# Kernel tuning notes

Measured on AMD Instinct MI355X. Metric: run time of the kernel, lower is better.

Reference implementation:

```python
import jax, jax.numpy as jnp
import numpy as np

S, B, DI, DH, NH = 1024, 64, 256, 256, 4  # seq_len, batch, input_dim, hidden_dim, attn_heads


def _lin(k, fan_in, shape):
    bound = 1.0 / np.sqrt(fan_in)
    return jax.random.uniform(k, shape, jnp.float32, -bound, bound)


def setup_inputs() -> dict:
    key = jax.random.key(0)
    ks = jax.random.split(key, 14)
    inp = {"inputs": jax.random.normal(ks[0], (S, B, DI), jnp.float32)}
    names = ["Wf", "bf", "Wi", "bi", "Wg", "bg", "Wo", "bo"]
    for j in range(4):
        inp[names[2 * j]] = _lin(ks[1 + 2 * j], DI + DH, (DI + DH, DH))
        inp[names[2 * j + 1]] = _lin(ks[2 + 2 * j], DI + DH, (DH,))
    inp["in_proj_w"] = _lin(ks[9], DH, (DH, 3 * DH))
    inp["in_proj_b"] = jnp.zeros((3 * DH,), jnp.float32)
    inp["out_proj_w"] = _lin(ks[10], DH, (DH, DH))
    inp["out_proj_b"] = jnp.zeros((DH,), jnp.float32)
    return inp


def reference(inputs, Wf, bf, Wi, bi, Wg, bg, Wo, bo,
              in_proj_w, in_proj_b, out_proj_w, out_proj_b):
    D = Wf.shape[1]
    bsz = inputs.shape[1]

    def step(carry, x):
        hx, cx = carry
        comb = jnp.concatenate([x, hx], axis=-1)  # [B, DI+DH]
        f = jax.nn.sigmoid(comb @ Wf + bf)
        i = jax.nn.sigmoid(comb @ Wi + bi)
        g = jnp.tanh(comb @ Wg + bg)
        o = jax.nn.sigmoid(comb @ Wo + bo)
        cx = f * cx + i * g
        hx = o * jnp.tanh(cx)
        return (hx, cx), hx

    init = (jnp.zeros((bsz, D), inputs.dtype), jnp.zeros((bsz, D), inputs.dtype))
    (hx, cx), Hseq = jax.lax.scan(step, init, inputs)  # Hseq: [S, B, D]

    # Faithful quirk: nn.MultiheadAttention(batch_first=True) is fed the
    # time-major [S, B, D] tensor, so S acts as the batch dim and attention
    # runs over the B (batch) axis.
    dh = D // NH
    qkv = Hseq @ in_proj_w + in_proj_b  # [S, B, 3D]
    q, k, v = jnp.split(qkv, 3, axis=-1)
    q = q.reshape(S_, bsz, NH, dh) if False else q.reshape(q.shape[0], bsz, NH, dh)
    k = k.reshape(k.shape[0], bsz, NH, dh)
    v = v.reshape(v.shape[0], bsz, NH, dh)
    scale = float(1.0 / np.sqrt(dh))
    scores = jnp.einsum('sqhd,skhd->shqk', q, k) * scale  # [S, H, B, B]
    attn = jax.nn.softmax(scores, axis=-1)
    ctx = jnp.einsum('shqk,skhd->sqhd', attn, v).reshape(Hseq.shape)
    attn_out = ctx @ out_proj_w + out_proj_b
    fused = Hseq + attn_out
    return (fused, (hx, cx))
```

## Files before the change

kernel.cpp:

```cpp
#include <hip/hip_runtime.h>
#include <cstdint>
#include <cstddef>


typedef _Float16 f16;
typedef __attribute__((ext_vector_type(2))) _Float16 half2v;
typedef __attribute__((ext_vector_type(4))) _Float16 half4v;
typedef __attribute__((ext_vector_type(8))) _Float16 half8v;
typedef __attribute__((ext_vector_type(4))) float   float4v;
typedef __attribute__((ext_vector_type(2))) float   float2v;

static __device__ __forceinline__ half2v u2h(unsigned u) {
  union { unsigned u; half2v h; } x; x.u = u; return x.h;
}
static __device__ __forceinline__ float sigm(float x) {
  return 1.0f / (1.0f + __expf(-x));
}
static __device__ __forceinline__ float tanh_fast(float x) {
  x = fminf(15.0f, fmaxf(-15.0f, x));
  float e = __expf(2.0f * x);
  return (e - 1.0f) / (e + 1.0f);
}
static __device__ __forceinline__ const float* selW(int g, const float* a, const float* b,
                                                    const float* c, const float* d) {
  return g == 0 ? a : (g == 1 ? b : (g == 2 ? c : d));
}

static __device__ __forceinline__ void wg_barrier_lds() {
  __builtin_amdgcn_sched_barrier(0);
  asm volatile("s_waitcnt lgkmcnt(0)" ::: "memory");
  __builtin_amdgcn_s_barrier();
  __builtin_amdgcn_sched_barrier(0);
}

__global__ void prep_k(const float* __restrict__ Wf, const float* __restrict__ Wi,
                       const float* __restrict__ Wg_, const float* __restrict__ Wo,
                       const float* __restrict__ bf, const float* __restrict__ bi,
                       const float* __restrict__ bg_, const float* __restrict__ bo,
                       const float* __restrict__ inpw, const float* __restrict__ outpw,
                       f16* __restrict__ wscan, f16* __restrict__ wxt,
                       f16* __restrict__ inpj, f16* __restrict__ outpj,
                       float* __restrict__ bias4)
{
  const int total = 262144 + 262144 + 196608 + 65536 + 1024;
  for (int e = blockIdx.x * blockDim.x + threadIdx.x; e < total; e += gridDim.x * blockDim.x) {
    int x = e;
    if (x < 262144) {
      int c = x >> 8, k = x & 255;
      int g = c >> 8, j = c & 255;
      const float* W = selW(g, Wf, Wi, Wg_, Wo);
      wscan[x] = (f16)W[(256 + k) * 256 + j];
      continue;
    }
    x -= 262144;
    if (x < 262144) {
      int j = x & 7, lane = (x >> 3) & 63, kstep = (x >> 9) & 7, ntile = x >> 12;
      int n = ntile * 16 + (lane & 15);
      int k = kstep * 32 + ((lane >> 4) & 3) * 8 + j;
      int g = n >> 8, jj = n & 255;
      const float* W = selW(g, Wf, Wi, Wg_, Wo);
      wxt[x] = (f16)W[k * 256 + jj];
      continue;
    }
    x -= 262144;
    if (x < 196608) {
      int j = x & 7, lane = (x >> 3) & 63, kstep = (x >> 9) & 7, ntile = x >> 12;
      int n = ntile * 16 + (lane & 15);
      int k = kstep * 32 + ((lane >> 4) & 3) * 8 + j;
      inpj[x] = (f16)inpw[k * 768 + n];
      continue;
    }
    x -= 196608;
    if (x < 65536) {
      int j = x & 7, lane = (x >> 3) & 63, kstep = (x >> 9) & 7, ntile = x >> 12;
      int n = ntile * 16 + (lane & 15);
      int k = kstep * 32 + ((lane >> 4) & 3) * 8 + j;
      outpj[x] = (f16)outpw[k * 256 + n];
      continue;
    }
    x -= 65536;
    {
      int g = x >> 8, j = x & 255;
      const float* bp = selW(g, bf, bi, bg_, bo);
      bias4[x] = bp[j];
    }
  }
}

__global__ void cvt_x_k(const float4v* __restrict__ X, half4v* __restrict__ Xh)
{
  int i = blockIdx.x * 256 + threadIdx.x;
  float4v v = X[i];
  half4v h;
  h.x = (f16)v.x; h.y = (f16)v.y; h.z = (f16)v.z; h.w = (f16)v.w;
  Xh[i] = h;
}

template<int NTOT, bool OUT_EPI>
__global__ __launch_bounds__(256, 2) void gemm_k(const f16* __restrict__ A,
    const f16* __restrict__ Bf, const float* __restrict__ bias,
    f16* __restrict__ Oh, float* __restrict__ Of)
{
  __shared__ f16 Al[8192];
  const int tid = threadIdx.x;
  const int lane = tid & 63;
  const int wm = (tid >> 7) & 1;
  const int wn = (tid >> 6) & 1;
  const int m0 = blockIdx.y * 128, n0 = blockIdx.x * 128;

  float4v acc[4][4];
  #pragma unroll
  for (int i = 0; i < 4; ++i)
    #pragma unroll
    for (int j = 0; j < 4; ++j) { acc[i][j].x = 0.f; acc[i][j].y = 0.f; acc[i][j].z = 0.f; acc[i][j].w = 0.f; }

  #pragma unroll 1
  for (int kc = 0; kc < 4; ++kc) {
    __syncthreads();
    #pragma unroll
    for (int p = 0; p < 4; ++p) {
      int m = p * 32 + (tid >> 3);
      int kk = (tid & 7) * 8;
      half8v v = *(const half8v*)(A + (size_t)(m0 + m) * 256 + kc * 64 + kk);
      int lt = ((kk >> 3) & 3) * 16 + (m & 15);
      *(half8v*)(Al + (((m >> 4) * 2 + (kk >> 5)) * 64 + lt) * 8) = v;
    }
    __syncthreads();
    half8v bfr[4][2], afr[4][2];
    #pragma unroll
    for (int i = 0; i < 4; ++i) {
      int NT = (n0 >> 4) + wn * 4 + i;
      #pragma unroll
      for (int ks = 0; ks < 2; ++ks)
        bfr[i][ks] = *(const half8v*)(Bf + (size_t)((NT * 8 + kc * 2 + ks) * 64 + lane) * 8);
    }
    #pragma unroll
    for (int i = 0; i < 4; ++i) {
      int MT = wm * 4 + i;
      #pragma unroll
      for (int ks = 0; ks < 2; ++ks)
        afr[i][ks] = *(const half8v*)(Al + ((MT * 2 + ks) * 64 + lane) * 8);
    }
    #pragma unroll
    for (int ks = 0; ks < 2; ++ks)
      #pragma unroll
      for (int i = 0; i < 4; ++i)
        #pragma unroll
        for (int jn = 0; jn < 4; ++jn)
          acc[i][jn] = __builtin_amdgcn_mfma_f32_16x16x32_f16(afr[i][ks], bfr[jn][ks], acc[i][jn], 0, 0, 0);
  }

  const int r0 = (lane >> 4) * 4, cn = lane & 15;
  #pragma unroll
  for (int i = 0; i < 4; ++i) {
    #pragma unroll
    for (int jn = 0; jn < 4; ++jn) {
      int n = n0 + wn * 64 + jn * 16 + cn;
      float bv = bias[n];
      int mb = m0 + wm * 64 + i * 16 + r0;
      #pragma unroll
      for (int r = 0; r < 4; ++r) {
        float v = acc[i][jn][r] + bv;
        size_t off = (size_t)(mb + r) * NTOT + n;
        if constexpr (OUT_EPI) Of[off] = v + Of[off];
        else                   Oh[off] = (f16)v;
      }
    }
  }
}

__global__ __launch_bounds__(512, 2) void scan_k(const f16* __restrict__ Xp,
    const f16* __restrict__ Wscan, float* __restrict__ dout, f16* __restrict__ Hh)
{
  extern __shared__ unsigned smem[];
  unsigned* wtl = smem;
  f16* hxs = (f16*)(smem + 32768);
  float* gts = (float*)(smem + 32768 + 128);
  const int tid = threadIdx.x;
  const int b = blockIdx.x;
  const int c0 = tid << 1;
  const unsigned* W32 = (const unsigned*)Wscan;

  unsigned wv[192];
  #pragma unroll
  for (int r = 0; r < 96; ++r) {
    wv[r]      = W32[c0 * 128 + r];
    wv[96 + r] = W32[(c0 + 1) * 128 + r];
  }
  for (int e = tid; e < 32768; e += 512) {
    int r2 = e >> 10, c = e & 1023;
    wtl[(r2 << 10) + c] = W32[c * 128 + 96 + r2];
  }
  if (tid < 128) ((unsigned*)hxs)[tid] = 0u;
  float cx = 0.0f, hx_keep = 0.0f;
  const int gate = tid >> 7;
  __syncthreads();

  const unsigned* xptr = (const unsigned*)Xp + (size_t)b * 512 + tid;
  unsigned xp_cur = xptr[0];

  #pragma unroll 1
  for (int t = 0; t < 1024; ++t) {
    unsigned xp_nxt = 0u;
    if (t + 1 < 1024) xp_nxt = xptr[(size_t)(t + 1) << 15];

    float a0 = 0.0f, a1 = 0.0f;
    #pragma unroll
    for (int ch = 0; ch < 24; ++ch) {
      half8v h8 = *(const half8v*)(hxs + ch * 8);
      const half2v* hp = (const half2v*)&h8;
      #pragma unroll
      for (int z = 0; z < 4; ++z) {
        int r = ch * 4 + z;
        a0 = __builtin_amdgcn_fdot2(hp[z], u2h(wv[r]), a0, false);
        a1 = __builtin_amdgcn_fdot2(hp[z], u2h(wv[96 + r]), a1, false);
      }
    }
    #pragma unroll
    for (int ch = 0; ch < 8; ++ch) {
      half8v h8 = *(const half8v*)(hxs + 192 + ch * 8);
      const half2v* hp = (const half2v*)&h8;
      #pragma unroll
      for (int z = 0; z < 4; ++z) {
        int r2 = ch * 4 + z;
        uint2 ww = *(const uint2*)(wtl + (r2 << 10) + c0);
        a0 = __builtin_amdgcn_fdot2(hp[z], u2h(ww.x), a0, false);
        a1 = __builtin_amdgcn_fdot2(hp[z], u2h(ww.y), a1, false);
      }
    }
    half2v xph = u2h(xp_cur);
    float p0 = a0 + (float)xph.x;
    float p1 = a1 + (float)xph.y;
    float v0, v1;
    if (gate == 2) { v0 = tanh_fast(p0); v1 = tanh_fast(p1); }
    else           { v0 = sigm(p0);      v1 = sigm(p1); }
    float2v gv; gv.x = v0; gv.y = v1;
    *(float2v*)(gts + c0) = gv;
    wg_barrier_lds();
    if (tid < 256) {
      float fg = gts[tid], ig = gts[256 + tid], gg = gts[512 + tid], og = gts[768 + tid];
      cx = fg * cx + ig * gg;
      float hv = og * tanh_fast(cx);
      hx_keep = hv;
      hxs[tid] = (f16)hv;
      size_t off = (size_t)(t * 64 + b) * 256 + tid;
      dout[off] = hv;
      Hh[off] = (f16)hv;
    }
    wg_barrier_lds();
    xp_cur = xp_nxt;
  }
  if (tid < 256) {
    dout[(size_t)16777216 + b * 256 + tid] = hx_keep;
    dout[(size_t)16777216 + 16384 + b * 256 + tid] = cx;
  }
}

__global__ __launch_bounds__(256, 2) void attn_k(const f16* __restrict__ qkv,
                                                 f16* __restrict__ ctx)
{
  __shared__ f16 ql[64 * 72];
  __shared__ f16 kl[64 * 72];
  __shared__ f16 vT[64 * 72];
  __shared__ f16 at[64 * 72];
  __shared__ float sc[64 * 69];
  __shared__ float pmx[256], psm[256], rmx[64], rsm[64];
  const int tid = threadIdx.x;
  const int s = blockIdx.x >> 2, h = blockIdx.x & 3;
  {
    const int bb = tid >> 2, i = tid & 3;
    const f16* base = qkv + (size_t)(s * 64 + bb) * 768 + h * 64 + i * 16;
    half8v q0 = *(const half8v*)(base);
    half8v q1 = *(const half8v*)(base + 8);
    *(half8v*)(ql + bb * 72 + i * 16)     = q0;
    *(half8v*)(ql + bb * 72 + i * 16 + 8) = q1;
    half8v k0 = *(const half8v*)(base + 256);
    half8v k1 = *(const half8v*)(base + 264);
    *(half8v*)(kl + bb * 72 + i * 16)     = k0;
    *(half8v*)(kl + bb * 72 + i * 16 + 8) = k1;
    half8v v0 = *(const half8v*)(base + 512);
    half8v v1 = *(const half8v*)(base + 520);
    #pragma unroll
    for (int z = 0; z < 8; ++z) {
      vT[(i * 16 + z) * 72 + bb]     = v0[z];
      vT[(i * 16 + 8 + z) * 72 + bb] = v1[z];
    }
  }
  __syncthreads();
  {
    const int qb = tid >> 2, g = tid & 3;
    half8v qr[8];
    #pragma unroll
    for (int i = 0; i < 8; ++i) qr[i] = *(const half8v*)(ql + qb * 72 + i * 8);
    #pragma unroll 1
    for (int jj = 0; jj < 16; ++jj) {
      int kb = g + jj * 4;
      float a = 0.0f;
      #pragma unroll
      for (int i = 0; i < 8; ++i) {
        half8v kr = *(const half8v*)(kl + kb * 72 + i * 8);
        const half2v* kp = (const half2v*)&kr;
        const half2v* qp = (const half2v*)&qr[i];
        #pragma unroll
        for (int z = 0; z < 4; ++z) a = __builtin_amdgcn_fdot2(qp[z], kp[z], a, false);
      }
      sc[qb * 69 + kb] = a * 0.125f;
    }
  }
  __syncthreads();
  {
    const int r = tid & 63, q = tid >> 6;
    float m = -1e30f;
    #pragma unroll
    for (int z = 0; z < 16; ++z) m = fmaxf(m, sc[r * 69 + q * 16 + z]);
    pmx[q * 64 + r] = m;
  }
  __syncthreads();
  if (tid < 64)
    rmx[tid] = fmaxf(fmaxf(pmx[tid], pmx[64 + tid]), fmaxf(pmx[128 + tid], pmx[192 + tid]));
  __syncthreads();
  {
    const int r = tid & 63, q = tid >> 6;
    float mx = rmx[r], ssum = 0.0f;
    #pragma unroll
    for (int z = 0; z < 16; ++z) {
      float e = __expf(sc[r * 69 + q * 16 + z] - mx);
      ssum += e;
      at[r * 72 + q * 16 + z] = (f16)e;
    }
    psm[q * 64 + r] = ssum;
  }
  __syncthreads();
  if (tid < 64)
    rsm[tid] = (psm[tid] + psm[64 + tid]) + (psm[128 + tid] + psm[192 + tid]);
  __syncthreads();
  {
    const int qb = tid >> 2, g = tid & 3;
    half8v ar[8];
    #pragma unroll
    for (int i = 0; i < 8; ++i) ar[i] = *(const half8v*)(at + qb * 72 + i * 8);
    const float rinv = 1.0f / rsm[qb];
    f16* outp = ctx + (size_t)(s * 64 + qb) * 256 + h * 64;
    #pragma unroll 1
    for (int z = 0; z < 16; ++z) {
      int d = g + z * 4;
      float a = 0.0f;
      #pragma unroll
      for (int i = 0; i < 8; ++i) {
        half8v vr = *(const half8v*)(vT + d * 72 + i * 8);
        const half2v* vp = (const half2v*)&vr;
        const half2v* ap = (const half2v*)&ar[i];
        #pragma unroll
        for (int zz = 0; zz < 4; ++zz) a = __builtin_amdgcn_fdot2(ap[zz], vp[zz], a, false);
      }
      outp[d] = (f16)(a * rinv);
    }
  }
}

extern "C" void kernel_launch(void* const* d_in, const int* in_sizes, int n_in,
                              void* d_out, int out_size, void* d_ws, size_t ws_size,
                              hipStream_t stream)
{
  (void)in_sizes; (void)n_in; (void)out_size; (void)ws_size;
  const float* X    = (const float*)d_in[0];
  const float* Wf   = (const float*)d_in[1];
  const float* bf   = (const float*)d_in[2];
  const float* Wi   = (const float*)d_in[3];
  const float* bi   = (const float*)d_in[4];
  const float* Wg   = (const float*)d_in[5];
  const float* bg   = (const float*)d_in[6];
  const float* Wo   = (const float*)d_in[7];
  const float* bo   = (const float*)d_in[8];
  const float* inpw = (const float*)d_in[9];
  const float* inpb = (const float*)d_in[10];
  const float* outpw= (const float*)d_in[11];
  const float* outpb= (const float*)d_in[12];

  char* ws = (char*)d_ws;
  f16*   Xp    = (f16*)(ws + 0);
  f16*   qkv   = (f16*)(ws + 0);
  f16*   ctxh  = (f16*)(ws + 100663296);
  f16*   Xh    = (f16*)(ws + 134217728);
  f16*   Hh    = (f16*)(ws + 167772160);
  f16*   wscan = (f16*)(ws + 201326592);
  f16*   wxt   = (f16*)(ws + 201850880);
  f16*   inpj  = (f16*)(ws + 202375168);
  f16*   outpj = (f16*)(ws + 202768384);
  float* bias4 = (float*)(ws + 202899456);
  float* out   = (float*)d_out;

  prep_k<<<1024, 256, 0, stream>>>(Wf, Wi, Wg, Wo, bf, bi, bg, bo, inpw, outpw,
                                   wscan, wxt, inpj, outpj, bias4);
  cvt_x_k<<<16384, 256, 0, stream>>>((const float4v*)X, (half4v*)Xh);
  gemm_k<1024, false><<<dim3(8, 512), 256, 0, stream>>>(Xh, wxt, bias4, Xp, nullptr);
  scan_k<<<64, 512, 135680, stream>>>(Xp, wscan, out, Hh);
  gemm_k<768, false><<<dim3(6, 512), 256, 0, stream>>>(Hh, inpj, inpb, qkv, nullptr);
  attn_k<<<4096, 256, 0, stream>>>(qkv, ctxh);
  gemm_k<256, true><<<dim3(2, 512), 256, 0, stream>>>(ctxh, outpj, outpb, nullptr, out);
}
```

Measured before the change: 2.680 ms.

## Use 1024 threads per scan block, one gate column per thread

The LSTM scan kernel now runs 1024 threads per batch row, each computing one gate column instead of two. This halves per-thread register weights (96 words) and shortens the serial dot-product chain per step. The LDS-resident part of the weights is relaid out into swizzled 16-byte chunks so each thread does one vector LDS read per chunk. Sigmoid and tanh switch from division to a hardware reciprocal. Doubling the threads adds wave-scheduling and barrier cost per step, and the launch_bounds change may force register spills.

```diff
diff --git a/kernel.cpp b/kernel.cpp
--- a/kernel.cpp
+++ b/kernel.cpp
@@ -9,17 +9,21 @@
 typedef __attribute__((ext_vector_type(8))) _Float16 half8v;
 typedef __attribute__((ext_vector_type(4))) float   float4v;
 typedef __attribute__((ext_vector_type(2))) float   float2v;
+typedef __attribute__((ext_vector_type(4))) unsigned uint4v;
 
 static __device__ __forceinline__ half2v u2h(unsigned u) {
   union { unsigned u; half2v h; } x; x.u = u; return x.h;
 }
+static __device__ __forceinline__ float rcp_fast(float x) {
+  return __builtin_amdgcn_rcpf(x);
+}
 static __device__ __forceinline__ float sigm(float x) {
-  return 1.0f / (1.0f + __expf(-x));
+  return rcp_fast(1.0f + __expf(-x));
 }
 static __device__ __forceinline__ float tanh_fast(float x) {
   x = fminf(15.0f, fmaxf(-15.0f, x));
   float e = __expf(2.0f * x);
-  return (e - 1.0f) / (e + 1.0f);
+  return (e - 1.0f) * rcp_fast(e + 1.0f);
 }
 static __device__ __forceinline__ const float* selW(int g, const float* a, const float* b,
                                                     const float* c, const float* d) {
@@ -169,73 +173,64 @@
   }
 }
 
-__global__ __launch_bounds__(512, 2) void scan_k(const f16* __restrict__ Xp,
+__global__ __launch_bounds__(1024, 4) void scan_k(const f16* __restrict__ Xp,
     const f16* __restrict__ Wscan, float* __restrict__ dout, f16* __restrict__ Hh)
 {
   extern __shared__ unsigned smem[];
-  unsigned* wtl = smem;
+  unsigned* wl = smem;
   f16* hxs = (f16*)(smem + 32768);
   float* gts = (float*)(smem + 32768 + 128);
   const int tid = threadIdx.x;
   const int b = blockIdx.x;
-  const int c0 = tid << 1;
+  const int c = tid;
+  const int gate = tid >> 8;
   const unsigned* W32 = (const unsigned*)Wscan;
 
-  unsigned wv[192];
+  unsigned wv[96];
   #pragma unroll
-  for (int r = 0; r < 96; ++r) {
-    wv[r]      = W32[c0 * 128 + r];
-    wv[96 + r] = W32[(c0 + 1) * 128 + r];
-  }
-  for (int e = tid; e < 32768; e += 512) {
-    int r2 = e >> 10, c = e & 1023;
-    wtl[(r2 << 10) + c] = W32[c * 128 + 96 + r2];
+  for (int r = 0; r < 96; ++r) wv[r] = W32[c * 128 + r];
+
+  const int cs = c ^ ((c >> 3) & 3);
+  #pragma unroll
+  for (int q4 = 0; q4 < 8; ++q4) {
+    uint4v w4 = *(const uint4v*)(W32 + c * 128 + 96 + q4 * 4);
+    *(uint4v*)(wl + q4 * 4096 + cs * 4) = w4;
   }
   if (tid < 128) ((unsigned*)hxs)[tid] = 0u;
   float cx = 0.0f, hx_keep = 0.0f;
-  const int gate = tid >> 7;
-  __syncthreads();
-
-  const unsigned* xptr = (const unsigned*)Xp + (size_t)b * 512 + tid;
-  unsigned xp_cur = xptr[0];
+  __syncthreads();
+
+  const f16* xptr = Xp + (size_t)b * 1024 + c;
+  f16 xp_cur = xptr[0];
 
   #pragma unroll 1
   for (int t = 0; t < 1024; ++t) {
-    unsigned xp_nxt = 0u;
-    if (t + 1 < 1024) xp_nxt = xptr[(size_t)(t + 1) << 15];
+    f16 xp_nxt = (f16)0.0f;
+    if (t + 1 < 1024) xp_nxt = xptr[(size_t)(t + 1) << 16];
 
     float a0 = 0.0f, a1 = 0.0f;
     #pragma unroll
     for (int ch = 0; ch < 24; ++ch) {
       half8v h8 = *(const half8v*)(hxs + ch * 8);
       const half2v* hp = (const half2v*)&h8;
-      #pragma unroll
-      for (int z = 0; z < 4; ++z) {
-        int r = ch * 4 + z;
-        a0 = __builtin_amdgcn_fdot2(hp[z], u2h(wv[r]), a0, false);
-        a1 = __builtin_amdgcn_fdot2(hp[z], u2h(wv[96 + r]), a1, false);
-      }
-    }
-    #pragma unroll
-    for (int ch = 0; ch < 8; ++ch) {
-      half8v h8 = *(const half8v*)(hxs + 192 + ch * 8);
+      a0 = __builtin_amdgcn_fdot2(hp[0], u2h(wv[ch * 4 + 0]), a0, false);
+      a1 = __builtin_amdgcn_fdot2(hp[1], u2h(wv[ch * 4 + 1]), a1, false);
+      a0 = __builtin_amdgcn_fdot2(hp[2], u2h(wv[ch * 4 + 2]), a0, false);
+      a1 = __builtin_amdgcn_fdot2(hp[3], u2h(wv[ch * 4 + 3]), a1, false);
+    }
+    #pragma unroll
+    for (int q4 = 0; q4 < 8; ++q4) {
+      half8v h8 = *(const half8v*)(hxs + 192 + q4 * 8);
       const half2v* hp = (const half2v*)&h8;
-      #pragma unroll
-      for (int z = 0; z < 4; ++z) {
-        int r2 = ch * 4 + z;
-        uint2 ww = *(const uint2*)(wtl + (r2 << 10) + c0);
-        a0 = __builtin_amdgcn_fdot2(hp[z], u2h(ww.x), a0, false);
-        a1 = __builtin_amdgcn_fdot2(hp[z], u2h(ww.y), a1, false);
-      }
-    }
-    half2v xph = u2h(xp_cur);
-    float p0 = a0 + (float)xph.x;
-    float p1 = a1 + (float)xph.y;
-    float v0, v1;
-    if (gate == 2) { v0 = tanh_fast(p0); v1 = tanh_fast(p1); }
-    else           { v0 = sigm(p0);      v1 = sigm(p1); }
-    float2v gv; gv.x = v0; gv.y = v1;
-    *(float2v*)(gts + c0) = gv;
+      uint4v ww = *(const uint4v*)(wl + q4 * 4096 + cs * 4);
+      a0 = __builtin_amdgcn_fdot2(hp[0], u2h(ww.x), a0, false);
+      a1 = __builtin_amdgcn_fdot2(hp[1], u2h(ww.y), a1, false);
+      a0 = __builtin_amdgcn_fdot2(hp[2], u2h(ww.z), a0, false);
+      a1 = __builtin_amdgcn_fdot2(hp[3], u2h(ww.w), a1, false);
+    }
+    float p = (a0 + a1) + (float)xp_cur;
+    float v = (gate == 2) ? tanh_fast(p) : sigm(p);
+    gts[c] = v;
     wg_barrier_lds();
     if (tid < 256) {
       float fg = gts[tid], ig = gts[256 + tid], gg = gts[512 + tid], og = gts[768 + tid];
@@ -394,7 +389,7 @@
                                    wscan, wxt, inpj, outpj, bias4);
   cvt_x_k<<<16384, 256, 0, stream>>>((const float4v*)X, (half4v*)Xh);
   gemm_k<1024, false><<<dim3(8, 512), 256, 0, stream>>>(Xh, wxt, bias4, Xp, nullptr);
-  scan_k<<<64, 512, 135680, stream>>>(Xp, wscan, out, Hh);
+  scan_k<<<64, 1024, 135680, stream>>>(Xp, wscan, out, Hh);
   gemm_k<768, false><<<dim3(6, 512), 256, 0, stream>>>(Hh, inpj, inpb, qkv, nullptr);
   attn_k<<<4096, 256, 0, stream>>>(qkv, ctxh);
   gemm_k<256, true><<<dim3(2, 512), 256, 0, stream>>>(ctxh, outpj, outpb, nullptr, out);
```

Result: slower. 3.718 ms (+38.8%).
